# Performance work log

Hardware: AMD Instinct MI355X
Metric: run time of the kernel (lower is better)

Reference implementation:

```python
import jax, jax.numpy as jnp
import numpy as np

# dims (must match init_kwargs / input_specs)
B_SZ = 1024
STOCH = 1024
ACT = 32
DETER = 4096
TOKENS = 8
TOKEN_DIM = DETER // TOKENS          # 512
EXPAND = 2
HIDDEN = EXPAND * TOKEN_DIM          # 1024
NHEADS = 8
HEADDIM = HIDDEN // NHEADS           # 128
DSTATE = 64
K = 4                                # conv kernel
LAYERS = 2
CONV_DIM = HIDDEN + 2 * DSTATE       # 1152
IN_PROJ_DIM = HIDDEN + CONV_DIM + NHEADS
EPS = 1e-4


def rmsnorm(x, w):
    return x * jax.lax.rsqrt(jnp.mean(x * x, axis=-1, keepdims=True) + EPS) * w


def silu(x):
    return x * jax.nn.sigmoid(x)


def setup_inputs() -> dict:
    key = jax.random.key(0)
    ks = jax.random.split(key, 16)

    def lin(k, shape, fan_in):
        return jax.random.normal(k, shape, jnp.float32) / np.sqrt(fan_in)

    # dt_bias init (inverse softplus of log-uniform dt in [1e-3, 1e-1])
    u = jax.random.uniform(ks[0], (LAYERS, NHEADS))
    dt = jnp.exp(u * (np.log(0.1) - np.log(0.001)) + np.log(0.001))
    dt = jnp.maximum(dt, 1e-4)
    dt_bias = dt + jnp.log(-jnp.expm1(-dt))

    return {
        "stoch": jax.random.normal(ks[1], (B_SZ, STOCH), jnp.float32),
        "deter": jax.random.normal(ks[2], (B_SZ, DETER), jnp.float32),
        "action": jax.random.normal(ks[3], (B_SZ, ACT), jnp.float32),
        "conv_state": jax.random.normal(ks[4], (LAYERS, B_SZ, CONV_DIM, K - 1), jnp.float32),
        "ssm_state": jax.random.normal(ks[5], (LAYERS, B_SZ, NHEADS, HEADDIM, DSTATE), jnp.float32),
        # input_proj: Linear(stoch+act -> token_dim) + RMSNorm + SiLU
        "in_proj_w": lin(ks[6], (TOKEN_DIM, STOCH + ACT), STOCH + ACT),
        "in_proj_b": jnp.zeros((TOKEN_DIM,), jnp.float32),
        "in_norm_w": jnp.ones((TOKEN_DIM,), jnp.float32),
        # per-block params, stacked over layers
        "blk_norm_w": jnp.ones((LAYERS, TOKEN_DIM), jnp.float32),
        "blk_in_w": lin(ks[7], (LAYERS, IN_PROJ_DIM, TOKEN_DIM), TOKEN_DIM),
        "blk_conv_w": lin(ks[8], (LAYERS, CONV_DIM, K), K),
        "blk_conv_b": jnp.zeros((LAYERS, CONV_DIM), jnp.float32),
        "blk_A_log": jnp.log(jax.random.uniform(ks[9], (LAYERS, NHEADS), minval=1.0, maxval=16.0)),
        "blk_D": jnp.ones((LAYERS, NHEADS), jnp.float32),
        "blk_dt_bias": dt_bias.astype(jnp.float32),
        "blk_post_norm_w": jnp.ones((LAYERS, HIDDEN), jnp.float32),
        "blk_out_w": lin(ks[10], (LAYERS, TOKEN_DIM, HIDDEN), HIDDEN),
        "blk_out_b": jnp.zeros((LAYERS, TOKEN_DIM), jnp.float32),
        "out_norm_w": jnp.ones((TOKEN_DIM,), jnp.float32),
    }


def reference(stoch, deter, action, conv_state, ssm_state,
              in_proj_w, in_proj_b, in_norm_w,
              blk_norm_w, blk_in_w, blk_conv_w, blk_conv_b,
              blk_A_log, blk_D, blk_dt_bias, blk_post_norm_w,
              blk_out_w, blk_out_b, out_norm_w):
    b = action.shape[0]
    # action normalization with detached denominator
    action = action / jax.lax.stop_gradient(jnp.maximum(jnp.abs(action), 1.0))
    inp = jnp.concatenate([stoch.reshape(b, -1), action], axis=-1)
    tok = silu(rmsnorm(inp @ in_proj_w.T + in_proj_b, in_norm_w))  # (B, token_dim)

    def block_step(x, layer):
        nw, iw, cw, cb, alog, dskip, dtb, pw, ow, ob, cs, ss = layer
        h = rmsnorm(x, nw)
        proj = h @ iw.T  # (B, hidden + conv_dim + nheads)
        z = proj[:, :HIDDEN]
        xBC = proj[:, HIDDEN:HIDDEN + CONV_DIM]
        dt_raw = proj[:, HIDDEN + CONV_DIM:]
        # depthwise causal conv on xBC with persistent state
        seq = jnp.concatenate([cs, xBC[:, :, None]], axis=-1)  # (B, conv_dim, K)
        conv = silu(jnp.einsum('ck,bck->bc', cw, seq) + cb)
        new_cs = seq[:, :, 1:]
        x_post = conv[:, :HIDDEN]
        Bp = conv[:, HIDDEN:HIDDEN + DSTATE]
        Cp = conv[:, HIDDEN + DSTATE:]
        xh = x_post.reshape(b, NHEADS, HEADDIM)
        # SSD single-step recurrence
        dt = jax.nn.softplus(dt_raw + dtb)           # (B, H)
        dA = jnp.exp(dt * (-jnp.exp(alog)))          # (B, H)
        dBx = jnp.einsum('bh,bn,bhp->bhpn', dt, Bp, xh)
        new_ss = ss * dA[:, :, None, None] + dBx     # (B, H, P, N)
        y = jnp.einsum('bhpn,bn->bhp', new_ss, Cp) + dskip[None, :, None] * xh
        gated = rmsnorm(y.reshape(b, HIDDEN) * silu(z), pw)
        out = gated @ ow.T + ob
        return x + out, (new_cs, new_ss)

    layers = (blk_norm_w, blk_in_w, blk_conv_w, blk_conv_b, blk_A_log, blk_D,
              blk_dt_bias, blk_post_norm_w, blk_out_w, blk_out_b,
              conv_state, ssm_state)
    x_final, (new_conv_state, new_ssm_state) = jax.lax.scan(block_step, tok, layers)

    x_t = rmsnorm(x_final, out_norm_w)  # (B, token_dim)
    # rolling tape of last TOKENS final-block outputs
    tape = deter.reshape(b, TOKENS, TOKEN_DIM)
    new_deter = jnp.concatenate([tape[:, 1:], x_t[:, None, :]], axis=1).reshape(b, DETER)
    return (new_deter, new_conv_state, new_ssm_state)
```

## Files before the change

### kernel.cpp

```cpp
#include <hip/hip_runtime.h>
#include <hip/hip_bf16.h>
#include <math.h>

#define B_SZ 1024
#define STOCH 1024
#define ACT 32
#define DETER 4096
#define TOKEN_DIM 512
#define HIDDEN 1024
#define NHEADS 8
#define HEADDIM 128
#define DSTATE 64
#define CONV_DIM 1152
#define IN_PROJ_DIM 2184
#define IPP 2240
#define KIN 1088
#define EPS 0.0001f

typedef float f32x4 __attribute__((ext_vector_type(4)));
typedef __bf16 bf16x8 __attribute__((ext_vector_type(8)));
typedef __bf16 bf16x4 __attribute__((ext_vector_type(4)));

#define N0C (512 * KIN / 4)
#define N1C (2 * IPP * TOKEN_DIM / 4)
#define N2C (2 * TOKEN_DIM * HIDDEN / 4)
__global__ __launch_bounds__(256) void prep_weights(
    const float* __restrict__ inproj, const float* __restrict__ blkin,
    const float* __restrict__ blkout,
    __bf16* __restrict__ w0, __bf16* __restrict__ w1, __bf16* __restrict__ w2)
{
    int i = blockIdx.x * 256 + threadIdx.x;
    bf16x4 o = { (__bf16)0.f, (__bf16)0.f, (__bf16)0.f, (__bf16)0.f };
    if (i < N0C) {
        int idx = i * 4;
        int rr = idx / KIN, cc = idx % KIN;
        if (cc < STOCH + ACT) {
            float4 v = *(const float4*)(inproj + (size_t)rr * (STOCH + ACT) + cc);
            o = bf16x4{ (__bf16)v.x, (__bf16)v.y, (__bf16)v.z, (__bf16)v.w };
        }
        ((bf16x4*)w0)[i] = o;
    } else if (i < N0C + N1C) {
        int j = i - N0C;
        int idx = j * 4;
        int li  = idx / (IPP * TOKEN_DIM);
        int rem = idx % (IPP * TOKEN_DIM);
        int rr  = rem / TOKEN_DIM, cc = rem % TOKEN_DIM;
        if (rr < IN_PROJ_DIM) {
            float4 v = *(const float4*)(blkin + ((size_t)li * IN_PROJ_DIM + rr) * TOKEN_DIM + cc);
            o = bf16x4{ (__bf16)v.x, (__bf16)v.y, (__bf16)v.z, (__bf16)v.w };
        }
        ((bf16x4*)w1)[j] = o;
    } else if (i < N0C + N1C + N2C) {
        int j = i - N0C - N1C;
        float4 v = ((const float4*)blkout)[j];
        o = bf16x4{ (__bf16)v.x, (__bf16)v.y, (__bf16)v.z, (__bf16)v.w };
        ((bf16x4*)w2)[j] = o;
    }
}

__global__ __launch_bounds__(256) void gemm_bf16_sw(
    const __bf16* __restrict__ A,
    const __bf16* __restrict__ W,
    const float* __restrict__ bias,
    const float* __restrict__ add,
    float* __restrict__ C,
    int M, int N, int K)
{
    __shared__ __bf16 As[64 * 64];
    __shared__ __bf16 Ws[64 * 64];
    const int tid = threadIdx.x;
    const int bm = blockIdx.y * 64;
    const int bn = blockIdx.x * 64;
    const int wid = tid >> 6;
    const int lane = tid & 63;
    const int wr = (wid >> 1) * 32;
    const int wc = (wid & 1) * 32;
    const int r = lane & 15;
    const int g16 = (lane >> 4) * 16;

    const int row0 = tid >> 3;
    const int colb = (tid * 16) & 0x70;
    const int wof0 = row0 * 128 + (colb ^ ((row0 & 7) << 4));
    const int wof1 = wof0 + 32 * 128;

    const __bf16* ga0 = A + (size_t)(bm + row0) * K + (colb >> 1);
    const __bf16* ga1 = ga0 + (size_t)32 * K;
    const __bf16* gw0 = W + (size_t)(bn + row0) * K + (colb >> 1);
    const __bf16* gw1 = gw0 + (size_t)32 * K;

    const int arow = wr + r;
    const int brow = wc + r;
    const int aswz = (arow & 7) << 4;
    const int bswz = (brow & 7) << 4;
    char* Asb = (char*)As;
    char* Wsb = (char*)Ws;

    f32x4 acc[2][2] = {};
    bf16x8 va0 = *(const bf16x8*)ga0;
    bf16x8 va1 = *(const bf16x8*)ga1;
    bf16x8 vw0 = *(const bf16x8*)gw0;
    bf16x8 vw1 = *(const bf16x8*)gw1;

    const int nsteps = K >> 6;
    for (int s = 0; s < nsteps; ++s) {
        __syncthreads();
        *(bf16x8*)(Asb + wof0) = va0;
        *(bf16x8*)(Asb + wof1) = va1;
        *(bf16x8*)(Wsb + wof0) = vw0;
        *(bf16x8*)(Wsb + wof1) = vw1;
        __syncthreads();
        if (s + 1 < nsteps) {
            const int ko = (s + 1) << 6;
            va0 = *(const bf16x8*)(ga0 + ko);
            va1 = *(const bf16x8*)(ga1 + ko);
            vw0 = *(const bf16x8*)(gw0 + ko);
            vw1 = *(const bf16x8*)(gw1 + ko);
        }
        #pragma unroll
        for (int ks = 0; ks < 2; ++ks) {
            const int cb = ks * 64 + g16;
            bf16x8 a0 = *(const bf16x8*)(Asb + arow * 128 + (cb ^ aswz));
            bf16x8 a1 = *(const bf16x8*)(Asb + (arow + 16) * 128 + (cb ^ aswz));
            bf16x8 b0 = *(const bf16x8*)(Wsb + brow * 128 + (cb ^ bswz));
            bf16x8 b1 = *(const bf16x8*)(Wsb + (brow + 16) * 128 + (cb ^ bswz));
            acc[0][0] = __builtin_amdgcn_mfma_f32_16x16x32_bf16(a0, b0, acc[0][0], 0, 0, 0);
            acc[0][1] = __builtin_amdgcn_mfma_f32_16x16x32_bf16(a0, b1, acc[0][1], 0, 0, 0);
            acc[1][0] = __builtin_amdgcn_mfma_f32_16x16x32_bf16(a1, b0, acc[1][0], 0, 0, 0);
            acc[1][1] = __builtin_amdgcn_mfma_f32_16x16x32_bf16(a1, b1, acc[1][1], 0, 0, 0);
        }
    }

    const int cr = (lane >> 4) * 4;
    const int cc = lane & 15;
    #pragma unroll
    for (int mi = 0; mi < 2; mi++) {
        #pragma unroll
        for (int ni = 0; ni < 2; ni++) {
            int n = bn + wc + ni * 16 + cc;
            #pragma unroll
            for (int j = 0; j < 4; j++) {
                int m = bm + wr + mi * 16 + cr + j;
                float v = acc[mi][ni][j];
                if (bias) v += bias[n];
                if (add)  v += add[(size_t)m * N + n];
                C[(size_t)m * N + n] = v;
            }
        }
    }
}

template<int D, bool SILU, typename OutT>
__global__ __launch_bounds__(256) void rmsnorm_kernel(
    const float* __restrict__ x, const float* __restrict__ w, OutT* __restrict__ out)
{
    constexpr int VPT = D / 256;
    int b = blockIdx.x;
    const float* row = x + (size_t)b * D;
    float v[VPT];
    float ss = 0.f;
    #pragma unroll
    for (int i = 0; i < VPT; i++) {
        v[i] = row[threadIdx.x + i * 256];
        ss += v[i] * v[i];
    }
    #pragma unroll
    for (int off = 32; off >= 1; off >>= 1) ss += __shfl_xor(ss, off);
    __shared__ float red[4];
    if ((threadIdx.x & 63) == 0) red[threadIdx.x >> 6] = ss;
    __syncthreads();
    float tot = red[0] + red[1] + red[2] + red[3];
    float scale = rsqrtf(tot / (float)D + EPS);
    OutT* orow = out + (size_t)b * D;
    #pragma unroll
    for (int i = 0; i < VPT; i++) {
        float val = v[i] * scale * w[threadIdx.x + i * 256];
        if (SILU) val = val / (1.f + expf(-val));
        orow[threadIdx.x + i * 256] = (OutT)val;
    }
}

__global__ __launch_bounds__(256) void gate_rmsnorm_kernel(
    const float* __restrict__ y, const float* __restrict__ proj,
    const float* __restrict__ pw, __bf16* __restrict__ out)
{
    int b = blockIdx.x;
    const float* yr = y + (size_t)b * HIDDEN;
    const float* zr = proj + (size_t)b * IPP;
    float v[4];
    float ss = 0.f;
    #pragma unroll
    for (int i = 0; i < 4; i++) {
        int j = threadIdx.x + i * 256;
        float z = zr[j];
        float val = yr[j] * (z / (1.f + expf(-z)));
        v[i] = val;
        ss += val * val;
    }
    #pragma unroll
    for (int off = 32; off >= 1; off >>= 1) ss += __shfl_xor(ss, off);
    __shared__ float red[4];
    if ((threadIdx.x & 63) == 0) red[threadIdx.x >> 6] = ss;
    __syncthreads();
    float tot = red[0] + red[1] + red[2] + red[3];
    float scale = rsqrtf(tot / (float)HIDDEN + EPS);
    __bf16* orow = out + (size_t)b * HIDDEN;
    #pragma unroll
    for (int i = 0; i < 4; i++) {
        int j = threadIdx.x + i * 256;
        orow[j] = (__bf16)(v[i] * scale * pw[j]);
    }
}

__global__ __launch_bounds__(256) void prep_inp_kernel(
    const float* __restrict__ stoch, const float* __restrict__ action, __bf16* __restrict__ inp)
{
    int idx = blockIdx.x * 256 + threadIdx.x;
    if (idx >= B_SZ * KIN) return;
    int b = idx / KIN;
    int j = idx - b * KIN;
    float v = 0.f;
    if (j < STOCH) {
        v = stoch[(size_t)b * STOCH + j];
    } else if (j < STOCH + ACT) {
        float a = action[(size_t)b * ACT + (j - STOCH)];
        float m = fabsf(a);
        v = a / (m > 1.f ? m : 1.f);
    }
    inp[idx] = (__bf16)v;
}

__global__ __launch_bounds__(256) void conv_kernel(
    const float* __restrict__ cs,
    const float* __restrict__ proj,
    const float* __restrict__ cw,
    const float* __restrict__ cb,
    float* __restrict__ convout,
    float* __restrict__ new_cs)
{
    int idx = blockIdx.x * 256 + threadIdx.x;
    if (idx >= B_SZ * CONV_DIM) return;
    int b = idx / CONV_DIM;
    int c = idx - b * CONV_DIM;
    const float* s = cs + ((size_t)b * CONV_DIM + c) * 3;
    float s0 = s[0], s1 = s[1], s2 = s[2];
    float xbc = proj[(size_t)b * IPP + HIDDEN + c];
    const float* wv = cw + c * 4;
    float v = wv[0] * s0 + wv[1] * s1 + wv[2] * s2 + wv[3] * xbc + cb[c];
    v = v / (1.f + expf(-v));
    convout[idx] = v;
    float* nc = new_cs + ((size_t)b * CONV_DIM + c) * 3;
    nc[0] = s1; nc[1] = s2; nc[2] = xbc;
}

__global__ __launch_bounds__(256) void ssm_kernel(
    const float* __restrict__ ss,
    const float* __restrict__ conv,
    const float* __restrict__ proj,
    const float* __restrict__ dtb,
    const float* __restrict__ alog,
    const float* __restrict__ Dv,
    float* __restrict__ new_ss,
    float* __restrict__ y)
{
    int b = blockIdx.x >> 3;
    int h = blockIdx.x & 7;
    int t = threadIdx.x;

    float dtr = proj[(size_t)b * IPP + HIDDEN + CONV_DIM + h] + dtb[h];
    float dt = dtr > 20.f ? dtr : log1pf(expf(dtr));
    float dA = expf(dt * -expf(alog[h]));
    float Dk = Dv[h];

    __shared__ float Bs[DSTATE], Cs[DSTATE];
    if (t < DSTATE) Bs[t] = conv[(size_t)b * CONV_DIM + HIDDEN + t];
    else if (t < 2 * DSTATE) Cs[t - DSTATE] = conv[(size_t)b * CONV_DIM + HIDDEN + DSTATE + (t - DSTATE)];
    __syncthreads();

    const int p0 = t >> 4;
    const int nq = (t & 15) * 4;
    float4 Bv = *(const float4*)&Bs[nq];
    float4 Cv = *(const float4*)&Cs[nq];

    const float* basep = ss + ((size_t)b * NHEADS + h) * HEADDIM * DSTATE;
    float* baseo = new_ss + ((size_t)b * NHEADS + h) * HEADDIM * DSTATE;
    const float* xrow = conv + (size_t)b * CONV_DIM + h * HEADDIM;
    float* yrow = y + (size_t)b * HIDDEN + h * HEADDIM;

    #pragma unroll
    for (int it = 0; it < 8; ++it) {
        int p = it * 16 + p0;
        float xp = xrow[p];
        float dtx = dt * xp;
        float4 s4 = *(const float4*)(basep + (size_t)p * DSTATE + nq);
        float4 o;
        o.x = fmaf(s4.x, dA, dtx * Bv.x);
        o.y = fmaf(s4.y, dA, dtx * Bv.y);
        o.z = fmaf(s4.z, dA, dtx * Bv.z);
        o.w = fmaf(s4.w, dA, dtx * Bv.w);
        *(float4*)(baseo + (size_t)p * DSTATE + nq) = o;
        float acc = o.x * Cv.x + o.y * Cv.y + o.z * Cv.z + o.w * Cv.w;
        acc += __shfl_xor(acc, 1);
        acc += __shfl_xor(acc, 2);
        acc += __shfl_xor(acc, 4);
        acc += __shfl_xor(acc, 8);
        if ((t & 15) == 0) yrow[p] = acc + Dk * xp;
    }
}

__global__ __launch_bounds__(256) void final_kernel(
    const float* __restrict__ X, const float* __restrict__ w,
    const float* __restrict__ deter, float* __restrict__ out)
{
    int b = blockIdx.x;
    int t = threadIdx.x;
    float v0 = X[(size_t)b * TOKEN_DIM + t];
    float v1 = X[(size_t)b * TOKEN_DIM + 256 + t];
    float ss = v0 * v0 + v1 * v1;
    #pragma unroll
    for (int off = 32; off >= 1; off >>= 1) ss += __shfl_xor(ss, off);
    __shared__ float red[4];
    if ((t & 63) == 0) red[t >> 6] = ss;
    __syncthreads();
    float tot = red[0] + red[1] + red[2] + red[3];
    float scale = rsqrtf(tot / (float)TOKEN_DIM + EPS);
    out[(size_t)b * DETER + 3584 + t] = v0 * scale * w[t];
    out[(size_t)b * DETER + 3584 + 256 + t] = v1 * scale * w[256 + t];
    const float4* src = (const float4*)(deter + (size_t)b * DETER + TOKEN_DIM);
    float4* dst = (float4*)(out + (size_t)b * DETER);
    #pragma unroll
    for (int j = 0; j < 4; ++j) {
        int idx = t + j * 256;
        if (idx < 896) dst[idx] = src[idx];
    }
}

extern "C" void kernel_launch(void* const* d_in, const int* in_sizes, int n_in,
                              void* d_out, int out_size, void* d_ws, size_t ws_size,
                              hipStream_t stream) {
    const float* stoch      = (const float*)d_in[0];
    const float* deter      = (const float*)d_in[1];
    const float* action     = (const float*)d_in[2];
    const float* conv_state = (const float*)d_in[3];
    const float* ssm_state  = (const float*)d_in[4];
    const float* in_proj_w  = (const float*)d_in[5];
    const float* in_proj_b  = (const float*)d_in[6];
    const float* in_norm_w  = (const float*)d_in[7];
    const float* blk_norm_w = (const float*)d_in[8];
    const float* blk_in_w   = (const float*)d_in[9];
    const float* blk_conv_w = (const float*)d_in[10];
    const float* blk_conv_b = (const float*)d_in[11];
    const float* blk_A_log  = (const float*)d_in[12];
    const float* blk_D      = (const float*)d_in[13];
    const float* blk_dt_bias= (const float*)d_in[14];
    const float* blk_post_norm_w = (const float*)d_in[15];
    const float* blk_out_w  = (const float*)d_in[16];
    const float* blk_out_b  = (const float*)d_in[17];
    const float* out_norm_w = (const float*)d_in[18];

    float* out_deter = (float*)d_out;
    float* out_cs    = out_deter + (size_t)B_SZ * DETER;
    float* out_ss    = out_cs + (size_t)2 * B_SZ * CONV_DIM * 3;

    char* ws = (char*)d_ws;
    __bf16* Wb_inproj = (__bf16*)ws;  ws += (size_t)TOKEN_DIM * KIN * 2;
    __bf16* Wb_blkin  = (__bf16*)ws;  ws += (size_t)2 * IPP * TOKEN_DIM * 2;
    __bf16* Wb_blkout = (__bf16*)ws;  ws += (size_t)2 * TOKEN_DIM * HIDDEN * 2;
    float*  X         = (float*)ws;   ws += (size_t)B_SZ * TOKEN_DIM * 4;
    __bf16* Hb        = (__bf16*)ws;  ws += (size_t)B_SZ * TOKEN_DIM * 2;
    float*  PROJ      = (float*)ws;   ws += (size_t)B_SZ * IPP * 4;
    float*  CONV      = (float*)ws;   ws += (size_t)B_SZ * CONV_DIM * 4;
    float*  Y         = (float*)ws;   ws += (size_t)B_SZ * HIDDEN * 4;
    __bf16* Gb        = (__bf16*)ws;  ws += (size_t)B_SZ * HIDDEN * 2;
    __bf16* INPb = (__bf16*)Y;

    {
        int total = N0C + N1C + N2C;
        prep_weights<<<(total + 255) / 256, 256, 0, stream>>>(
            in_proj_w, blk_in_w, blk_out_w, Wb_inproj, Wb_blkin, Wb_blkout);
    }
    {
        int n = B_SZ * KIN;
        prep_inp_kernel<<<(n + 255) / 256, 256, 0, stream>>>(stoch, action, INPb);
    }
    {
        dim3 grid(TOKEN_DIM / 64, B_SZ / 64);
        gemm_bf16_sw<<<grid, 256, 0, stream>>>(INPb, Wb_inproj, in_proj_b, nullptr, PROJ,
                                               B_SZ, TOKEN_DIM, KIN);
        rmsnorm_kernel<TOKEN_DIM, true, float><<<B_SZ, 256, 0, stream>>>(PROJ, in_norm_w, X);
    }

    for (int l = 0; l < 2; ++l) {
        const float* nw  = blk_norm_w + (size_t)l * TOKEN_DIM;
        const __bf16* iw = Wb_blkin + (size_t)l * IPP * TOKEN_DIM;
        const float* cw  = blk_conv_w + (size_t)l * CONV_DIM * 4;
        const float* cb  = blk_conv_b + (size_t)l * CONV_DIM;
        const float* alog= blk_A_log + (size_t)l * NHEADS;
        const float* Dv  = blk_D + (size_t)l * NHEADS;
        const float* dtb = blk_dt_bias + (size_t)l * NHEADS;
        const float* pw  = blk_post_norm_w + (size_t)l * HIDDEN;
        const __bf16* ow = Wb_blkout + (size_t)l * TOKEN_DIM * HIDDEN;
        const float* ob  = blk_out_b + (size_t)l * TOKEN_DIM;
        const float* cs_in = conv_state + (size_t)l * B_SZ * CONV_DIM * 3;
        const float* ss_in = ssm_state + (size_t)l * B_SZ * NHEADS * HEADDIM * DSTATE;
        float* cs_out = out_cs + (size_t)l * B_SZ * CONV_DIM * 3;
        float* ss_out = out_ss + (size_t)l * B_SZ * NHEADS * HEADDIM * DSTATE;

        rmsnorm_kernel<TOKEN_DIM, false, __bf16><<<B_SZ, 256, 0, stream>>>(X, nw, Hb);
        {
            dim3 grid(IPP / 64, B_SZ / 64);
            gemm_bf16_sw<<<grid, 256, 0, stream>>>(Hb, iw, nullptr, nullptr, PROJ,
                                                   B_SZ, IPP, TOKEN_DIM);
        }
        {
            int n = B_SZ * CONV_DIM;
            conv_kernel<<<(n + 255) / 256, 256, 0, stream>>>(cs_in, PROJ, cw, cb, CONV, cs_out);
        }
        ssm_kernel<<<B_SZ * NHEADS, 256, 0, stream>>>(ss_in, CONV, PROJ, dtb, alog, Dv, ss_out, Y);
        gate_rmsnorm_kernel<<<B_SZ, 256, 0, stream>>>(Y, PROJ, pw, Gb);
        {
            dim3 grid(TOKEN_DIM / 64, B_SZ / 64);
            gemm_bf16_sw<<<grid, 256, 0, stream>>>(Gb, ow, ob, X, X,
                                                   B_SZ, TOKEN_DIM, HIDDEN);
        }
    }

    final_kernel<<<B_SZ, 256, 0, stream>>>(X, out_norm_w, deter, out_deter);
}
```

Before: 330.8 us.

## Fuse conv/SSM/gate kernels, split-K small GEMMs with fused reduce+norm epilogues

Replaces the GEMM with a 128x64 tile variant and uses split-K (4 partial buffers) for the narrow in-proj and out-proj GEMMs. Reduce kernels then sum the partials and fuse bias, residual, RMSNorm/SiLU and the next layer's pre-norm or the final tape write. Conv, SSM recurrence and gated RMSNorm are merged into one per-batch kernel that keeps intermediates in shared memory. The projection width is padded to 2304, and the net effect is fewer launches and less intermediate global traffic. The cost is extra partial-sum buffer traffic, and the SSM stage now runs with fewer blocks (one per batch row) doing all heads serially.

```diff
diff --git a/kernel.cpp b/kernel.cpp
--- a/kernel.cpp
+++ b/kernel.cpp
@@ -13,7 +13,7 @@
 #define DSTATE 64
 #define CONV_DIM 1152
 #define IN_PROJ_DIM 2184
-#define IPP 2240
+#define IPP2 2304
 #define KIN 1088
 #define EPS 0.0001f
 
@@ -22,7 +22,7 @@
 typedef __bf16 bf16x4 __attribute__((ext_vector_type(4)));
 
 #define N0C (512 * KIN / 4)
-#define N1C (2 * IPP * TOKEN_DIM / 4)
+#define N1C (2 * IPP2 * TOKEN_DIM / 4)
 #define N2C (2 * TOKEN_DIM * HIDDEN / 4)
 __global__ __launch_bounds__(256) void prep_weights(
     const float* __restrict__ inproj, const float* __restrict__ blkin,
@@ -42,8 +42,8 @@
     } else if (i < N0C + N1C) {
         int j = i - N0C;
         int idx = j * 4;
-        int li  = idx / (IPP * TOKEN_DIM);
-        int rem = idx % (IPP * TOKEN_DIM);
+        int li  = idx / (IPP2 * TOKEN_DIM);
+        int rem = idx % (IPP2 * TOKEN_DIM);
         int rr  = rem / TOKEN_DIM, cc = rem % TOKEN_DIM;
         if (rr < IN_PROJ_DIM) {
             float4 v = *(const float4*)(blkin + ((size_t)li * IN_PROJ_DIM + rr) * TOKEN_DIM + cc);
@@ -55,159 +55,6 @@
         float4 v = ((const float4*)blkout)[j];
         o = bf16x4{ (__bf16)v.x, (__bf16)v.y, (__bf16)v.z, (__bf16)v.w };
         ((bf16x4*)w2)[j] = o;
-    }
-}
-
-__global__ __launch_bounds__(256) void gemm_bf16_sw(
-    const __bf16* __restrict__ A,
-    const __bf16* __restrict__ W,
-    const float* __restrict__ bias,
-    const float* __restrict__ add,
-    float* __restrict__ C,
-    int M, int N, int K)
-{
-    __shared__ __bf16 As[64 * 64];
-    __shared__ __bf16 Ws[64 * 64];
-    const int tid = threadIdx.x;
-    const int bm = blockIdx.y * 64;
-    const int bn = blockIdx.x * 64;
-    const int wid = tid >> 6;
-    const int lane = tid & 63;
-    const int wr = (wid >> 1) * 32;
-    const int wc = (wid & 1) * 32;
-    const int r = lane & 15;
-    const int g16 = (lane >> 4) * 16;
-
-    const int row0 = tid >> 3;
-    const int colb = (tid * 16) & 0x70;
-    const int wof0 = row0 * 128 + (colb ^ ((row0 & 7) << 4));
-    const int wof1 = wof0 + 32 * 128;
-
-    const __bf16* ga0 = A + (size_t)(bm + row0) * K + (colb >> 1);
-    const __bf16* ga1 = ga0 + (size_t)32 * K;
-    const __bf16* gw0 = W + (size_t)(bn + row0) * K + (colb >> 1);
-    const __bf16* gw1 = gw0 + (size_t)32 * K;
-
-    const int arow = wr + r;
-    const int brow = wc + r;
-    const int aswz = (arow & 7) << 4;
-    const int bswz = (brow & 7) << 4;
-    char* Asb = (char*)As;
-    char* Wsb = (char*)Ws;
-
-    f32x4 acc[2][2] = {};
-    bf16x8 va0 = *(const bf16x8*)ga0;
-    bf16x8 va1 = *(const bf16x8*)ga1;
-    bf16x8 vw0 = *(const bf16x8*)gw0;
-    bf16x8 vw1 = *(const bf16x8*)gw1;
-
-    const int nsteps = K >> 6;
-    for (int s = 0; s < nsteps; ++s) {
-        __syncthreads();
-        *(bf16x8*)(Asb + wof0) = va0;
-        *(bf16x8*)(Asb + wof1) = va1;
-        *(bf16x8*)(Wsb + wof0) = vw0;
-        *(bf16x8*)(Wsb + wof1) = vw1;
-        __syncthreads();
-        if (s + 1 < nsteps) {
-            const int ko = (s + 1) << 6;
-            va0 = *(const bf16x8*)(ga0 + ko);
-            va1 = *(const bf16x8*)(ga1 + ko);
-            vw0 = *(const bf16x8*)(gw0 + ko);
-            vw1 = *(const bf16x8*)(gw1 + ko);
-        }
-        #pragma unroll
-        for (int ks = 0; ks < 2; ++ks) {
-            const int cb = ks * 64 + g16;
-            bf16x8 a0 = *(const bf16x8*)(Asb + arow * 128 + (cb ^ aswz));
-            bf16x8 a1 = *(const bf16x8*)(Asb + (arow + 16) * 128 + (cb ^ aswz));
-            bf16x8 b0 = *(const bf16x8*)(Wsb + brow * 128 + (cb ^ bswz));
-            bf16x8 b1 = *(const bf16x8*)(Wsb + (brow + 16) * 128 + (cb ^ bswz));
-            acc[0][0] = __builtin_amdgcn_mfma_f32_16x16x32_bf16(a0, b0, acc[0][0], 0, 0, 0);
-            acc[0][1] = __builtin_amdgcn_mfma_f32_16x16x32_bf16(a0, b1, acc[0][1], 0, 0, 0);
-            acc[1][0] = __builtin_amdgcn_mfma_f32_16x16x32_bf16(a1, b0, acc[1][0], 0, 0, 0);
-            acc[1][1] = __builtin_amdgcn_mfma_f32_16x16x32_bf16(a1, b1, acc[1][1], 0, 0, 0);
-        }
-    }
-
-    const int cr = (lane >> 4) * 4;
-    const int cc = lane & 15;
-    #pragma unroll
-    for (int mi = 0; mi < 2; mi++) {
-        #pragma unroll
-        for (int ni = 0; ni < 2; ni++) {
-            int n = bn + wc + ni * 16 + cc;
-            #pragma unroll
-            for (int j = 0; j < 4; j++) {
-                int m = bm + wr + mi * 16 + cr + j;
-                float v = acc[mi][ni][j];
-                if (bias) v += bias[n];
-                if (add)  v += add[(size_t)m * N + n];
-                C[(size_t)m * N + n] = v;
-            }
-        }
-    }
-}
-
-template<int D, bool SILU, typename OutT>
-__global__ __launch_bounds__(256) void rmsnorm_kernel(
-    const float* __restrict__ x, const float* __restrict__ w, OutT* __restrict__ out)
-{
-    constexpr int VPT = D / 256;
-    int b = blockIdx.x;
-    const float* row = x + (size_t)b * D;
-    float v[VPT];
-    float ss = 0.f;
-    #pragma unroll
-    for (int i = 0; i < VPT; i++) {
-        v[i] = row[threadIdx.x + i * 256];
-        ss += v[i] * v[i];
-    }
-    #pragma unroll
-    for (int off = 32; off >= 1; off >>= 1) ss += __shfl_xor(ss, off);
-    __shared__ float red[4];
-    if ((threadIdx.x & 63) == 0) red[threadIdx.x >> 6] = ss;
-    __syncthreads();
-    float tot = red[0] + red[1] + red[2] + red[3];
-    float scale = rsqrtf(tot / (float)D + EPS);
-    OutT* orow = out + (size_t)b * D;
-    #pragma unroll
-    for (int i = 0; i < VPT; i++) {
-        float val = v[i] * scale * w[threadIdx.x + i * 256];
-        if (SILU) val = val / (1.f + expf(-val));
-        orow[threadIdx.x + i * 256] = (OutT)val;
-    }
-}
-
-__global__ __launch_bounds__(256) void gate_rmsnorm_kernel(
-    const float* __restrict__ y, const float* __restrict__ proj,
-    const float* __restrict__ pw, __bf16* __restrict__ out)
-{
-    int b = blockIdx.x;
-    const float* yr = y + (size_t)b * HIDDEN;
-    const float* zr = proj + (size_t)b * IPP;
-    float v[4];
-    float ss = 0.f;
-    #pragma unroll
-    for (int i = 0; i < 4; i++) {
-        int j = threadIdx.x + i * 256;
-        float z = zr[j];
-        float val = yr[j] * (z / (1.f + expf(-z)));
-        v[i] = val;
-        ss += val * val;
-    }
-    #pragma unroll
-    for (int off = 32; off >= 1; off >>= 1) ss += __shfl_xor(ss, off);
-    __shared__ float red[4];
-    if ((threadIdx.x & 63) == 0) red[threadIdx.x >> 6] = ss;
-    __syncthreads();
-    float tot = red[0] + red[1] + red[2] + red[3];
-    float scale = rsqrtf(tot / (float)HIDDEN + EPS);
-    __bf16* orow = out + (size_t)b * HIDDEN;
-    #pragma unroll
-    for (int i = 0; i < 4; i++) {
-        int j = threadIdx.x + i * 256;
-        orow[j] = (__bf16)(v[i] * scale * pw[j]);
     }
 }
 
@@ -229,108 +76,306 @@
     inp[idx] = (__bf16)v;
 }
 
-__global__ __launch_bounds__(256) void conv_kernel(
+template<bool SPLIT>
+__global__ __launch_bounds__(256) void gemm_v2(
+    const __bf16* __restrict__ A,
+    const __bf16* __restrict__ W,
+    const float* __restrict__ bias,
+    float* __restrict__ C,
+    int M, int N, int K, int chunk_steps)
+{
+    __shared__ __bf16 As[128 * 64];
+    __shared__ __bf16 Ws[64 * 64];
+    const int tid = threadIdx.x;
+    const int bn = blockIdx.x * 64;
+    const int bm = blockIdx.y * 128;
+    const int nsteps = K >> 6;
+    int s_begin = 0, s_end = nsteps;
+    float* Cout = C;
+    if (SPLIT) {
+        int z = blockIdx.z;
+        s_begin = z * chunk_steps;
+        int se = s_begin + chunk_steps;
+        s_end = se < nsteps ? se : nsteps;
+        Cout = C + (size_t)z * M * N;
+    }
+
+    const int wid = tid >> 6;
+    const int lane = tid & 63;
+    const int wr = wid * 32;
+    const int r = lane & 15;
+    const int kb = (lane >> 4) * 16;
+
+    const int row0 = tid >> 3;
+    const int colb = (tid & 7) * 16;
+    const int wof = row0 * 128 + (colb ^ ((row0 & 7) << 4));
+    char* Asb = (char*)As;
+    char* Wsb = (char*)Ws;
+
+    const __bf16* gA = A + (size_t)(bm + row0) * K + (s_begin << 6) + (colb >> 1);
+    const __bf16* gW = W + (size_t)(bn + row0) * K + (s_begin << 6) + (colb >> 1);
+    const size_t aK32 = (size_t)32 * K;
+
+    const int ar0 = wr + r;
+    const int ar1 = wr + 16 + r;
+    const int aswz = (ar0 & 7) << 4;
+    const int bswz = (r & 7) << 4;
+
+    f32x4 acc[2][4] = {};
+    bf16x8 va0 = *(const bf16x8*)(gA);
+    bf16x8 va1 = *(const bf16x8*)(gA + aK32);
+    bf16x8 va2 = *(const bf16x8*)(gA + 2 * aK32);
+    bf16x8 va3 = *(const bf16x8*)(gA + 3 * aK32);
+    bf16x8 vw0 = *(const bf16x8*)(gW);
+    bf16x8 vw1 = *(const bf16x8*)(gW + aK32);
+
+    for (int s = s_begin; s < s_end; ++s) {
+        __syncthreads();
+        *(bf16x8*)(Asb + wof) = va0;
+        *(bf16x8*)(Asb + wof + 32 * 128) = va1;
+        *(bf16x8*)(Asb + wof + 64 * 128) = va2;
+        *(bf16x8*)(Asb + wof + 96 * 128) = va3;
+        *(bf16x8*)(Wsb + wof) = vw0;
+        *(bf16x8*)(Wsb + wof + 32 * 128) = vw1;
+        __syncthreads();
+        if (s + 1 < s_end) {
+            const int ko = (s + 1 - s_begin) << 6;
+            va0 = *(const bf16x8*)(gA + ko);
+            va1 = *(const bf16x8*)(gA + aK32 + ko);
+            va2 = *(const bf16x8*)(gA + 2 * aK32 + ko);
+            va3 = *(const bf16x8*)(gA + 3 * aK32 + ko);
+            vw0 = *(const bf16x8*)(gW + ko);
+            vw1 = *(const bf16x8*)(gW + aK32 + ko);
+        }
+        #pragma unroll
+        for (int ks = 0; ks < 2; ++ks) {
+            const int cb = ks * 64 + kb;
+            bf16x8 a0 = *(const bf16x8*)(Asb + ar0 * 128 + (cb ^ aswz));
+            bf16x8 a1 = *(const bf16x8*)(Asb + ar1 * 128 + (cb ^ aswz));
+            bf16x8 b0 = *(const bf16x8*)(Wsb + r * 128 + (cb ^ bswz));
+            bf16x8 b1 = *(const bf16x8*)(Wsb + (r + 16) * 128 + (cb ^ bswz));
+            bf16x8 b2 = *(const bf16x8*)(Wsb + (r + 32) * 128 + (cb ^ bswz));
+            bf16x8 b3 = *(const bf16x8*)(Wsb + (r + 48) * 128 + (cb ^ bswz));
+            acc[0][0] = __builtin_amdgcn_mfma_f32_16x16x32_bf16(a0, b0, acc[0][0], 0, 0, 0);
+            acc[0][1] = __builtin_amdgcn_mfma_f32_16x16x32_bf16(a0, b1, acc[0][1], 0, 0, 0);
+            acc[0][2] = __builtin_amdgcn_mfma_f32_16x16x32_bf16(a0, b2, acc[0][2], 0, 0, 0);
+            acc[0][3] = __builtin_amdgcn_mfma_f32_16x16x32_bf16(a0, b3, acc[0][3], 0, 0, 0);
+            acc[1][0] = __builtin_amdgcn_mfma_f32_16x16x32_bf16(a1, b0, acc[1][0], 0, 0, 0);
+            acc[1][1] = __builtin_amdgcn_mfma_f32_16x16x32_bf16(a1, b1, acc[1][1], 0, 0, 0);
+            acc[1][2] = __builtin_amdgcn_mfma_f32_16x16x32_bf16(a1, b2, acc[1][2], 0, 0, 0);
+            acc[1][3] = __builtin_amdgcn_mfma_f32_16x16x32_bf16(a1, b3, acc[1][3], 0, 0, 0);
+        }
+    }
+
+    const int cr = (lane >> 4) * 4;
+    const int cc = lane & 15;
+    #pragma unroll
+    for (int mi = 0; mi < 2; mi++) {
+        #pragma unroll
+        for (int ni = 0; ni < 4; ni++) {
+            int n = bn + ni * 16 + cc;
+            #pragma unroll
+            for (int j = 0; j < 4; j++) {
+                int m = bm + wr + mi * 16 + cr + j;
+                float v = acc[mi][ni][j];
+                if (!SPLIT && bias) v += bias[n];
+                Cout[(size_t)m * N + n] = v;
+            }
+        }
+    }
+}
+
+__device__ __forceinline__ float block_sum(float v, float* red, int t) {
+    #pragma unroll
+    for (int off = 32; off >= 1; off >>= 1) v += __shfl_xor(v, off);
+    if ((t & 63) == 0) red[t >> 6] = v;
+    __syncthreads();
+    float tot = red[0] + red[1] + red[2] + red[3];
+    __syncthreads();
+    return tot;
+}
+
+__global__ __launch_bounds__(256) void reduce_in_kernel(
+    const float* __restrict__ P,
+    const float* __restrict__ bias,
+    const float* __restrict__ inw,
+    const float* __restrict__ nw,
+    float* __restrict__ X, __bf16* __restrict__ Hb)
+{
+    __shared__ float red[4];
+    int b = blockIdx.x, t = threadIdx.x;
+    const size_t stride = (size_t)B_SZ * TOKEN_DIM;
+    float h[2];
+    float ss = 0.f;
+    #pragma unroll
+    for (int i = 0; i < 2; i++) {
+        int c = t + i * 256;
+        size_t o = (size_t)b * TOKEN_DIM + c;
+        float v = P[o] + P[o + stride] + P[o + 2 * stride] + P[o + 3 * stride] + bias[c];
+        h[i] = v;
+        ss += v * v;
+    }
+    float tot = block_sum(ss, red, t);
+    float sc = rsqrtf(tot / (float)TOKEN_DIM + EPS);
+    float ss2 = 0.f;
+    #pragma unroll
+    for (int i = 0; i < 2; i++) {
+        int c = t + i * 256;
+        float v = h[i] * sc * inw[c];
+        v = v / (1.f + expf(-v));
+        h[i] = v;
+        X[(size_t)b * TOKEN_DIM + c] = v;
+        ss2 += v * v;
+    }
+    float tot2 = block_sum(ss2, red, t);
+    float sc2 = rsqrtf(tot2 / (float)TOKEN_DIM + EPS);
+    #pragma unroll
+    for (int i = 0; i < 2; i++) {
+        int c = t + i * 256;
+        Hb[(size_t)b * TOKEN_DIM + c] = (__bf16)(h[i] * sc2 * nw[c]);
+    }
+}
+
+template<int MODE>
+__global__ __launch_bounds__(256) void reduce_out_kernel(
+    const float* __restrict__ P,
+    const float* __restrict__ ob,
+    const float* __restrict__ Xin,
+    const float* __restrict__ w,
+    float* __restrict__ X,
+    __bf16* __restrict__ Hb,
+    const float* __restrict__ deter,
+    float* __restrict__ out)
+{
+    __shared__ float red[4];
+    int b = blockIdx.x, t = threadIdx.x;
+    const size_t stride = (size_t)B_SZ * TOKEN_DIM;
+    float h[2];
+    float ss = 0.f;
+    #pragma unroll
+    for (int i = 0; i < 2; i++) {
+        int c = t + i * 256;
+        size_t o = (size_t)b * TOKEN_DIM + c;
+        float v = Xin[o] + P[o] + P[o + stride] + P[o + 2 * stride] + P[o + 3 * stride] + ob[c];
+        h[i] = v;
+        ss += v * v;
+    }
+    float tot = block_sum(ss, red, t);
+    float sc = rsqrtf(tot / (float)TOKEN_DIM + EPS);
+    if (MODE == 0) {
+        #pragma unroll
+        for (int i = 0; i < 2; i++) {
+            int c = t + i * 256;
+            size_t o = (size_t)b * TOKEN_DIM + c;
+            X[o] = h[i];
+            Hb[o] = (__bf16)(h[i] * sc * w[c]);
+        }
+    } else {
+        #pragma unroll
+        for (int i = 0; i < 2; i++) {
+            int c = t + i * 256;
+            out[(size_t)b * DETER + 3584 + c] = h[i] * sc * w[c];
+        }
+        const float4* src = (const float4*)(deter + (size_t)b * DETER + TOKEN_DIM);
+        float4* dst = (float4*)(out + (size_t)b * DETER);
+        #pragma unroll
+        for (int j = 0; j < 4; ++j) {
+            int idx = t + j * 256;
+            if (idx < 896) dst[idx] = src[idx];
+        }
+    }
+}
+
+__global__ __launch_bounds__(256) void conv_ssm_gate_kernel(
     const float* __restrict__ cs,
     const float* __restrict__ proj,
     const float* __restrict__ cw,
     const float* __restrict__ cb,
-    float* __restrict__ convout,
-    float* __restrict__ new_cs)
-{
-    int idx = blockIdx.x * 256 + threadIdx.x;
-    if (idx >= B_SZ * CONV_DIM) return;
-    int b = idx / CONV_DIM;
-    int c = idx - b * CONV_DIM;
-    const float* s = cs + ((size_t)b * CONV_DIM + c) * 3;
-    float s0 = s[0], s1 = s[1], s2 = s[2];
-    float xbc = proj[(size_t)b * IPP + HIDDEN + c];
-    const float* wv = cw + c * 4;
-    float v = wv[0] * s0 + wv[1] * s1 + wv[2] * s2 + wv[3] * xbc + cb[c];
-    v = v / (1.f + expf(-v));
-    convout[idx] = v;
-    float* nc = new_cs + ((size_t)b * CONV_DIM + c) * 3;
-    nc[0] = s1; nc[1] = s2; nc[2] = xbc;
-}
-
-__global__ __launch_bounds__(256) void ssm_kernel(
-    const float* __restrict__ ss,
-    const float* __restrict__ conv,
-    const float* __restrict__ proj,
     const float* __restrict__ dtb,
     const float* __restrict__ alog,
     const float* __restrict__ Dv,
+    const float* __restrict__ pw,
+    const float* __restrict__ ss,
+    float* __restrict__ new_cs,
     float* __restrict__ new_ss,
-    float* __restrict__ y)
-{
-    int b = blockIdx.x >> 3;
-    int h = blockIdx.x & 7;
-    int t = threadIdx.x;
-
-    float dtr = proj[(size_t)b * IPP + HIDDEN + CONV_DIM + h] + dtb[h];
-    float dt = dtr > 20.f ? dtr : log1pf(expf(dtr));
-    float dA = expf(dt * -expf(alog[h]));
-    float Dk = Dv[h];
-
-    __shared__ float Bs[DSTATE], Cs[DSTATE];
-    if (t < DSTATE) Bs[t] = conv[(size_t)b * CONV_DIM + HIDDEN + t];
-    else if (t < 2 * DSTATE) Cs[t - DSTATE] = conv[(size_t)b * CONV_DIM + HIDDEN + DSTATE + (t - DSTATE)];
+    __bf16* __restrict__ Gb)
+{
+    __shared__ float convs[CONV_DIM];
+    __shared__ float yrow[HIDDEN];
+    __shared__ float dts[NHEADS], dAs[NHEADS], dvs[NHEADS];
+    __shared__ float red[4];
+
+    int b = blockIdx.x, t = threadIdx.x;
+
+    if (t < NHEADS) {
+        float dtr = proj[(size_t)b * IPP2 + HIDDEN + CONV_DIM + t] + dtb[t];
+        float dt = dtr > 20.f ? dtr : log1pf(expf(dtr));
+        dts[t] = dt;
+        dAs[t] = expf(dt * -expf(alog[t]));
+        dvs[t] = Dv[t];
+    }
+    for (int c = t; c < CONV_DIM; c += 256) {
+        const float* s = cs + ((size_t)b * CONV_DIM + c) * 3;
+        float s0 = s[0], s1 = s[1], s2 = s[2];
+        float xbc = proj[(size_t)b * IPP2 + HIDDEN + c];
+        float4 wv = *(const float4*)(cw + c * 4);
+        float v = wv.x * s0 + wv.y * s1 + wv.z * s2 + wv.w * xbc + cb[c];
+        v = v / (1.f + expf(-v));
+        convs[c] = v;
+        float* nc = new_cs + ((size_t)b * CONV_DIM + c) * 3;
+        nc[0] = s1; nc[1] = s2; nc[2] = xbc;
+    }
     __syncthreads();
 
     const int p0 = t >> 4;
     const int nq = (t & 15) * 4;
-    float4 Bv = *(const float4*)&Bs[nq];
-    float4 Cv = *(const float4*)&Cs[nq];
-
-    const float* basep = ss + ((size_t)b * NHEADS + h) * HEADDIM * DSTATE;
-    float* baseo = new_ss + ((size_t)b * NHEADS + h) * HEADDIM * DSTATE;
-    const float* xrow = conv + (size_t)b * CONV_DIM + h * HEADDIM;
-    float* yrow = y + (size_t)b * HIDDEN + h * HEADDIM;
-
-    #pragma unroll
-    for (int it = 0; it < 8; ++it) {
-        int p = it * 16 + p0;
-        float xp = xrow[p];
-        float dtx = dt * xp;
-        float4 s4 = *(const float4*)(basep + (size_t)p * DSTATE + nq);
-        float4 o;
-        o.x = fmaf(s4.x, dA, dtx * Bv.x);
-        o.y = fmaf(s4.y, dA, dtx * Bv.y);
-        o.z = fmaf(s4.z, dA, dtx * Bv.z);
-        o.w = fmaf(s4.w, dA, dtx * Bv.w);
-        *(float4*)(baseo + (size_t)p * DSTATE + nq) = o;
-        float acc = o.x * Cv.x + o.y * Cv.y + o.z * Cv.z + o.w * Cv.w;
-        acc += __shfl_xor(acc, 1);
-        acc += __shfl_xor(acc, 2);
-        acc += __shfl_xor(acc, 4);
-        acc += __shfl_xor(acc, 8);
-        if ((t & 15) == 0) yrow[p] = acc + Dk * xp;
-    }
-}
-
-__global__ __launch_bounds__(256) void final_kernel(
-    const float* __restrict__ X, const float* __restrict__ w,
-    const float* __restrict__ deter, float* __restrict__ out)
-{
-    int b = blockIdx.x;
-    int t = threadIdx.x;
-    float v0 = X[(size_t)b * TOKEN_DIM + t];
-    float v1 = X[(size_t)b * TOKEN_DIM + 256 + t];
-    float ss = v0 * v0 + v1 * v1;
-    #pragma unroll
-    for (int off = 32; off >= 1; off >>= 1) ss += __shfl_xor(ss, off);
-    __shared__ float red[4];
-    if ((t & 63) == 0) red[t >> 6] = ss;
+    float4 Bv = *(const float4*)&convs[HIDDEN + nq];
+    float4 Cv = *(const float4*)&convs[HIDDEN + DSTATE + nq];
+    const float* basep = ss + (size_t)b * NHEADS * HEADDIM * DSTATE;
+    float* baseo = new_ss + (size_t)b * NHEADS * HEADDIM * DSTATE;
+
+    for (int h = 0; h < NHEADS; ++h) {
+        float dt = dts[h], dA = dAs[h], Dk = dvs[h];
+        const float* sp = basep + (size_t)h * HEADDIM * DSTATE;
+        float* op = baseo + (size_t)h * HEADDIM * DSTATE;
+        #pragma unroll
+        for (int it = 0; it < 8; ++it) {
+            int p = it * 16 + p0;
+            float xp = convs[h * HEADDIM + p];
+            float dtx = dt * xp;
+            float4 s4 = *(const float4*)(sp + (size_t)p * DSTATE + nq);
+            float4 o;
+            o.x = fmaf(s4.x, dA, dtx * Bv.x);
+            o.y = fmaf(s4.y, dA, dtx * Bv.y);
+            o.z = fmaf(s4.z, dA, dtx * Bv.z);
+            o.w = fmaf(s4.w, dA, dtx * Bv.w);
+            *(float4*)(op + (size_t)p * DSTATE + nq) = o;
+            float acc = o.x * Cv.x + o.y * Cv.y + o.z * Cv.z + o.w * Cv.w;
+            acc += __shfl_xor(acc, 1);
+            acc += __shfl_xor(acc, 2);
+            acc += __shfl_xor(acc, 4);
+            acc += __shfl_xor(acc, 8);
+            if ((t & 15) == 0) yrow[h * HEADDIM + p] = acc + Dk * xp;
+        }
+    }
     __syncthreads();
-    float tot = red[0] + red[1] + red[2] + red[3];
-    float scale = rsqrtf(tot / (float)TOKEN_DIM + EPS);
-    out[(size_t)b * DETER + 3584 + t] = v0 * scale * w[t];
-    out[(size_t)b * DETER + 3584 + 256 + t] = v1 * scale * w[256 + t];
-    const float4* src = (const float4*)(deter + (size_t)b * DETER + TOKEN_DIM);
-    float4* dst = (float4*)(out + (size_t)b * DETER);
-    #pragma unroll
-    for (int j = 0; j < 4; ++j) {
-        int idx = t + j * 256;
-        if (idx < 896) dst[idx] = src[idx];
+
+    float vv[4];
+    float ssum = 0.f;
+    #pragma unroll
+    for (int i = 0; i < 4; i++) {
+        int j = t + i * 256;
+        float z = proj[(size_t)b * IPP2 + j];
+        float val = yrow[j] * (z / (1.f + expf(-z)));
+        vv[i] = val;
+        ssum += val * val;
+    }
+    float tot = block_sum(ssum, red, t);
+    float sc = rsqrtf(tot / (float)HIDDEN + EPS);
+    #pragma unroll
+    for (int i = 0; i < 4; i++) {
+        int j = t + i * 256;
+        Gb[(size_t)b * HIDDEN + j] = (__bf16)(vv[i] * sc * pw[j]);
     }
 }
 
@@ -363,15 +408,14 @@
 
     char* ws = (char*)d_ws;
     __bf16* Wb_inproj = (__bf16*)ws;  ws += (size_t)TOKEN_DIM * KIN * 2;
-    __bf16* Wb_blkin  = (__bf16*)ws;  ws += (size_t)2 * IPP * TOKEN_DIM * 2;
+    __bf16* Wb_blkin  = (__bf16*)ws;  ws += (size_t)2 * IPP2 * TOKEN_DIM * 2;
     __bf16* Wb_blkout = (__bf16*)ws;  ws += (size_t)2 * TOKEN_DIM * HIDDEN * 2;
     float*  X         = (float*)ws;   ws += (size_t)B_SZ * TOKEN_DIM * 4;
     __bf16* Hb        = (__bf16*)ws;  ws += (size_t)B_SZ * TOKEN_DIM * 2;
-    float*  PROJ      = (float*)ws;   ws += (size_t)B_SZ * IPP * 4;
-    float*  CONV      = (float*)ws;   ws += (size_t)B_SZ * CONV_DIM * 4;
-    float*  Y         = (float*)ws;   ws += (size_t)B_SZ * HIDDEN * 4;
+    float*  PROJ      = (float*)ws;   ws += (size_t)B_SZ * IPP2 * 4;
     __bf16* Gb        = (__bf16*)ws;  ws += (size_t)B_SZ * HIDDEN * 2;
-    __bf16* INPb = (__bf16*)Y;
+    float*  PART      = (float*)ws;   ws += (size_t)4 * B_SZ * TOKEN_DIM * 4;
+    __bf16* INPb = (__bf16*)PROJ;
 
     {
         int total = N0C + N1C + N2C;
@@ -383,19 +427,19 @@
         prep_inp_kernel<<<(n + 255) / 256, 256, 0, stream>>>(stoch, action, INPb);
     }
     {
-        dim3 grid(TOKEN_DIM / 64, B_SZ / 64);
-        gemm_bf16_sw<<<grid, 256, 0, stream>>>(INPb, Wb_inproj, in_proj_b, nullptr, PROJ,
-                                               B_SZ, TOKEN_DIM, KIN);
-        rmsnorm_kernel<TOKEN_DIM, true, float><<<B_SZ, 256, 0, stream>>>(PROJ, in_norm_w, X);
+        dim3 grid(TOKEN_DIM / 64, B_SZ / 128, 4);
+        gemm_v2<true><<<grid, 256, 0, stream>>>(INPb, Wb_inproj, nullptr, PART,
+                                                B_SZ, TOKEN_DIM, KIN, 5);
+        reduce_in_kernel<<<B_SZ, 256, 0, stream>>>(PART, in_proj_b, in_norm_w,
+                                                   blk_norm_w, X, Hb);
     }
 
     for (int l = 0; l < 2; ++l) {
-        const float* nw  = blk_norm_w + (size_t)l * TOKEN_DIM;
-        const __bf16* iw = Wb_blkin + (size_t)l * IPP * TOKEN_DIM;
+        const __bf16* iw = Wb_blkin + (size_t)l * IPP2 * TOKEN_DIM;
         const float* cw  = blk_conv_w + (size_t)l * CONV_DIM * 4;
-        const float* cb  = blk_conv_b + (size_t)l * CONV_DIM;
+        const float* cbv = blk_conv_b + (size_t)l * CONV_DIM;
         const float* alog= blk_A_log + (size_t)l * NHEADS;
-        const float* Dv  = blk_D + (size_t)l * NHEADS;
+        const float* Dvv = blk_D + (size_t)l * NHEADS;
         const float* dtb = blk_dt_bias + (size_t)l * NHEADS;
         const float* pw  = blk_post_norm_w + (size_t)l * HIDDEN;
         const __bf16* ow = Wb_blkout + (size_t)l * TOKEN_DIM * HIDDEN;
@@ -405,24 +449,24 @@
         float* cs_out = out_cs + (size_t)l * B_SZ * CONV_DIM * 3;
         float* ss_out = out_ss + (size_t)l * B_SZ * NHEADS * HEADDIM * DSTATE;
 
-        rmsnorm_kernel<TOKEN_DIM, false, __bf16><<<B_SZ, 256, 0, stream>>>(X, nw, Hb);
         {
-            dim3 grid(IPP / 64, B_SZ / 64);
-            gemm_bf16_sw<<<grid, 256, 0, stream>>>(Hb, iw, nullptr, nullptr, PROJ,
-                                                   B_SZ, IPP, TOKEN_DIM);
-        }
+            dim3 grid(IPP2 / 64, B_SZ / 128);
+            gemm_v2<false><<<grid, 256, 0, stream>>>(Hb, iw, nullptr, PROJ,
+                                                     B_SZ, IPP2, TOKEN_DIM, 0);
+        }
+        conv_ssm_gate_kernel<<<B_SZ, 256, 0, stream>>>(
+            cs_in, PROJ, cw, cbv, dtb, alog, Dvv, pw, ss_in, cs_out, ss_out, Gb);
         {
-            int n = B_SZ * CONV_DIM;
-            conv_kernel<<<(n + 255) / 256, 256, 0, stream>>>(cs_in, PROJ, cw, cb, CONV, cs_out);
-        }
-        ssm_kernel<<<B_SZ * NHEADS, 256, 0, stream>>>(ss_in, CONV, PROJ, dtb, alog, Dv, ss_out, Y);
-        gate_rmsnorm_kernel<<<B_SZ, 256, 0, stream>>>(Y, PROJ, pw, Gb);
-        {
-            dim3 grid(TOKEN_DIM / 64, B_SZ / 64);
-            gemm_bf16_sw<<<grid, 256, 0, stream>>>(Gb, ow, ob, X, X,
-                                                   B_SZ, TOKEN_DIM, HIDDEN);
-        }
-    }
-
-    final_kernel<<<B_SZ, 256, 0, stream>>>(X, out_norm_w, deter, out_deter);
-}
+            dim3 grid(TOKEN_DIM / 64, B_SZ / 128, 4);
+            gemm_v2<true><<<grid, 256, 0, stream>>>(Gb, ow, nullptr, PART,
+                                                    B_SZ, TOKEN_DIM, HIDDEN, 4);
+        }
+        if (l == 0) {
+            reduce_out_kernel<0><<<B_SZ, 256, 0, stream>>>(
+                PART, ob, X, blk_norm_w + TOKEN_DIM, X, Hb, nullptr, nullptr);
+        } else {
+            reduce_out_kernel<1><<<B_SZ, 256, 0, stream>>>(
+                PART, ob, X, out_norm_w, nullptr, nullptr, deter, out_deter);
+        }
+    }
+}
```

Result: faster. 308.4 us (-6.8%).
